# Performance work log

Hardware: AMD Instinct MI355X
Metric: run time of the kernel (lower is better)

The kernel has to match this reference:

```python
import jax, jax.numpy as jnp
import numpy as np

LAMBDA_SCR = 0.015
LAMBDA_IFD = 0.015


def setup_inputs() -> dict:
    key = jax.random.key(0)
    k = jax.random.split(key, 5)
    pred = jax.random.normal(k[0], (32, 1000), dtype=jnp.float32)
    feat0 = jax.random.normal(k[1], (32, 64, 128, 128), dtype=jnp.float32)
    feat1 = jax.random.normal(k[2], (32, 128, 64, 64), dtype=jnp.float32)
    feat2 = jax.random.normal(k[3], (32, 256, 32, 32), dtype=jnp.float32)  # teacher
    target = jax.random.randint(k[4], (32,), 0, 1000, dtype=jnp.int64)
    return {"pred": pred, "feat0": feat0, "feat1": feat1, "feat2": feat2, "target": target}


def _adaptive_avg_pool2d(x, out_hw):
    # Exact-multiple adaptive average pool (matches torch for integer ratios).
    B, C, H, W = x.shape
    Ho, Wo = out_hw
    if Ho >= H:
        x = jnp.repeat(x, Ho // H, axis=2)  # replication upsample
    else:
        x = x.reshape(B, C, Ho, H // Ho, W).mean(axis=3)
    if Wo >= W:
        x = jnp.repeat(x, Wo // W, axis=3)
    else:
        x = x.reshape(B, C, x.shape[2], Wo, W // Wo).mean(axis=4)
    return x


def _random_channel_selection(feat, target_channels, key):
    C = feat.shape[1]
    if C == target_channels:
        return feat
    idx = jax.random.permutation(key, C)[:target_channels]
    return feat[:, idx, :, :]


def _ifd_loss(feat):
    B, C, H, W = feat.shape
    if C < 2:
        return jnp.float32(0.0)
    # L2 norm per channel -> descending sort of channel indices
    norms = jnp.linalg.norm(feat.reshape(B, C, H * W), axis=-1)  # [B, C]
    idx = jnp.argsort(-norms, axis=1)                            # [B, C]
    half = C // 2
    strong = jnp.take_along_axis(feat, idx[:, :half, None, None], axis=1)
    weak = jnp.take_along_axis(feat, idx[:, half:2 * half, None, None], axis=1)
    A_strong = jax.nn.sigmoid(strong.mean(axis=1))  # [B, H, W]
    A_weak = jax.nn.sigmoid(weak.mean(axis=1))
    # sum_b mean_hw(diff^2) / B == mean over all elements
    return jnp.mean((A_weak - jax.lax.stop_gradient(A_strong)) ** 2)


def reference(pred, feat0, feat1, feat2, target):
    logp = jax.nn.log_softmax(pred, axis=-1)
    l_main = -jnp.mean(jnp.take_along_axis(logp, target[:, None], axis=1))

    features = [feat0, feat1, feat2]
    teacher = features[-1]
    students = features[:-1]

    sel_key = jax.random.key(42)  # fixed keys stand in for torch.randperm
    l_scr = jnp.float32(0.0)
    for i, student in enumerate(students):
        t_down = _adaptive_avg_pool2d(teacher, student.shape[2:])
        min_C = min(teacher.shape[1], student.shape[1])
        ks, kt = jax.random.split(jax.random.fold_in(sel_key, i))
        s_aligned = _random_channel_selection(student, min_C, ks)
        t_aligned = _random_channel_selection(t_down, min_C, kt)
        l_scr = l_scr + jnp.mean((s_aligned - jax.lax.stop_gradient(t_aligned)) ** 2)
    l_scr = l_scr / len(students)

    l_ifd = jnp.float32(0.0)
    for feat in features:
        l_ifd = l_ifd + _ifd_loss(feat)
    l_ifd = l_ifd / len(features)

    total = l_main + LAMBDA_SCR * l_scr + LAMBDA_IFD * l_ifd
    return (total, l_main, l_scr, l_ifd)
```

## Files before the change

### kernel.cpp

```cpp
#include <hip/hip_runtime.h>
#include <stdint.h>
#include <math.h>

#define NB 32

__device__ __forceinline__ void tf_block(uint32_t k0, uint32_t k1, uint32_t& x0, uint32_t& x1) {
  uint32_t k2 = 0x1BD11BDAu ^ k0 ^ k1;
  x0 += k0; x1 += k1;
#define TFR(r) { x0 += x1; x1 = (x1 << r) | (x1 >> (32 - r)); x1 ^= x0; }
  TFR(13) TFR(15) TFR(26) TFR(6)
  x0 += k1; x1 += k2 + 1u;
  TFR(17) TFR(29) TFR(16) TFR(24)
  x0 += k2; x1 += k0 + 2u;
  TFR(13) TFR(15) TFR(26) TFR(6)
  x0 += k0; x1 += k1 + 3u;
  TFR(17) TFR(29) TFR(16) TFR(24)
  x0 += k1; x1 += k2 + 4u;
  TFR(13) TFR(15) TFR(26) TFR(6)
  x0 += k2; x1 += k0 + 5u;
#undef TFR
}

__device__ __forceinline__ float sigmoidf(float x) { return 1.0f / (1.0f + expf(-x)); }

__device__ __forceinline__ float block_reduce(float v, float* red) {
  __syncthreads();
  int lane = threadIdx.x & 63, wv = threadIdx.x >> 6;
  for (int o = 32; o > 0; o >>= 1) v += __shfl_down(v, o, 64);
  if (lane == 0) red[wv] = v;
  __syncthreads();
  float r = 0.f;
  if (threadIdx.x == 0) r = red[0] + red[1] + red[2] + red[3];
  return r;
}

__global__ __launch_bounds__(256) void k0_perm(int* idx0, int* idx1, float* ws) {
  __shared__ uint32_t sub[2][2];
  __shared__ uint32_t bits[2][256];
  int t = threadIdx.x;
  for (int i = t; i < 384; i += 256) ws[i] = 0.0f;
  if (t == 0) {
    for (int i = 0; i < 2; ++i) {
      uint32_t f0 = 0u, f1 = (uint32_t)i;
      tf_block(0u, 42u, f0, f1);
      uint32_t a0 = 0u, a1 = 2u; tf_block(f0, f1, a0, a1);
      uint32_t b0 = 1u, b1 = 3u; tf_block(f0, f1, b0, b1);
      uint32_t kt0 = a1, kt1 = b1;
      uint32_t c0 = 0u, c1 = 2u; tf_block(kt0, kt1, c0, c1);
      uint32_t d0 = 1u, d1 = 3u; tf_block(kt0, kt1, d0, d1);
      sub[i][0] = c1; sub[i][1] = d1;
    }
  }
  __syncthreads();
  if (t < 128) {
    for (int i = 0; i < 2; ++i) {
      uint32_t x0 = (uint32_t)t, x1 = (uint32_t)(t + 128);
      tf_block(sub[i][0], sub[i][1], x0, x1);
      bits[i][t] = x0; bits[i][t + 128] = x1;
    }
  }
  __syncthreads();
  for (int i = 0; i < 2; ++i) {
    uint32_t mine = bits[i][t];
    int rank = 0;
    for (int k = 0; k < 256; ++k) {
      uint32_t v = bits[i][k];
      rank += (v < mine) || (v == mine && k < t);
    }
    int lim = (i == 0) ? 64 : 128;
    if (rank < lim) { (i == 0 ? idx0 : idx1)[rank] = t; }
  }
}

template<int C, int HW, int LOGW, int SHIFT, bool STUDENT>
__device__ __forceinline__ void pass1_work(const float* __restrict__ feat,
                                           const float* __restrict__ teacher,
                                           const int* __restrict__ tidx,
                                           float* __restrict__ normsq,
                                           float* __restrict__ scr_slots,
                                           int bc, float* tpl, float* red) {
  if constexpr (STUDENT) {
    int b = bc / C, c = bc % C;
    int tc = tidx[c];
    ((float4*)tpl)[threadIdx.x] =
        ((const float4*)(teacher + ((size_t)b * 256 + tc) * 1024))[threadIdx.x];
    __syncthreads();
  }
  const float4* plane = (const float4*)(feat + (size_t)bc * HW);
  float ssq = 0.f, scr = 0.f;
  for (int p = threadIdx.x; p < HW / 4; p += 256) {
    float4 v = plane[p];
    ssq += v.x * v.x + v.y * v.y + v.z * v.z + v.w * v.w;
    if constexpr (STUDENT) {
      int pix = p * 4;
      int h = pix >> LOGW;
      int w = pix & ((1 << LOGW) - 1);
      int th = h >> SHIFT;
      if constexpr (SHIFT == 2) {
        float tv = tpl[th * 32 + (w >> 2)];
        float dx = v.x - tv, dy = v.y - tv, dz = v.z - tv, dw = v.w - tv;
        scr += dx * dx + dy * dy + dz * dz + dw * dw;
      } else {
        int tw = w >> 1;
        float t0 = tpl[th * 32 + tw], t1 = tpl[th * 32 + tw + 1];
        float dx = v.x - t0, dy = v.y - t0, dz = v.z - t1, dw = v.w - t1;
        scr += dx * dx + dy * dy + dz * dz + dw * dw;
      }
    }
  }
  float r = block_reduce(ssq, red);
  if (threadIdx.x == 0) normsq[bc] = r;
  if constexpr (STUDENT) {
    float r2 = block_reduce(scr, red);
    if (threadIdx.x == 0) atomicAdd(&scr_slots[bc & 63], r2);
  }
}

__global__ __launch_bounds__(256) void k1_pass1(
    const float* __restrict__ f0, const float* __restrict__ f1, const float* __restrict__ f2,
    const int* __restrict__ idx0, const int* __restrict__ idx1,
    float* __restrict__ ns0, float* __restrict__ ns1, float* __restrict__ ns2,
    float* __restrict__ scr0_s, float* __restrict__ scr1_s) {
  __shared__ float tpl[1024];
  __shared__ float red[8];
  int bid = blockIdx.x;
  if (bid < 2048)       pass1_work<64, 16384, 7, 2, true >(f0, f2, idx0, ns0, scr0_s, bid,        tpl, red);
  else if (bid < 6144)  pass1_work<128, 4096, 6, 1, true >(f1, f2, idx1, ns1, scr1_s, bid - 2048, tpl, red);
  else                  pass1_work<256, 1024, 5, 0, false>(f2, nullptr, nullptr, ns2, nullptr, bid - 6144, tpl, red);
}

template<int C>
__device__ __forceinline__ void rank_work(const float* __restrict__ normsq,
                                          float* __restrict__ flags, int b, float* nm) {
  for (int c = threadIdx.x; c < C; c += 256) nm[c] = sqrtf(normsq[b * C + c]);
  __syncthreads();
  for (int c = threadIdx.x; c < C; c += 256) {
    float mine = nm[c];
    int rank = 0;
    for (int k = 0; k < C; ++k) {
      float v = nm[k];
      rank += (v > mine) || (v == mine && k < c);
    }
    flags[b * C + c] = (rank < C / 2) ? 1.0f : 0.0f;
  }
}

__device__ __forceinline__ void main_work(const float* __restrict__ pred,
                                          const int* __restrict__ target,
                                          float* acc, int b, float* sh) {
  int t = threadIdx.x;
  const float* row = pred + b * 1000;
  float m = -INFINITY;
  for (int j = t; j < 1000; j += 256) m = fmaxf(m, row[j]);
  sh[t] = m; __syncthreads();
  for (int s = 128; s > 0; s >>= 1) { if (t < s) sh[t] = fmaxf(sh[t], sh[t + s]); __syncthreads(); }
  m = sh[0]; __syncthreads();
  float e = 0.f;
  for (int j = t; j < 1000; j += 256) e += expf(row[j] - m);
  sh[t] = e; __syncthreads();
  for (int s = 128; s > 0; s >>= 1) { if (t < s) sh[t] += sh[t + s]; __syncthreads(); }
  if (t == 0) atomicAdd(acc, (logf(sh[0]) + m - row[target[b]]) * (1.0f / 32.0f));
}

__global__ __launch_bounds__(256) void k2_rank_main(
    const float* __restrict__ ns0, const float* __restrict__ ns1, const float* __restrict__ ns2,
    float* __restrict__ fl0, float* __restrict__ fl1, float* __restrict__ fl2,
    const float* __restrict__ pred, const int* __restrict__ target, float* main_acc) {
  __shared__ float sh[256];
  int bid = blockIdx.x;
  if (bid < 32)       rank_work<64 >(ns0, fl0, bid,      sh);
  else if (bid < 64)  rank_work<128>(ns1, fl1, bid - 32, sh);
  else if (bid < 96)  rank_work<256>(ns2, fl2, bid - 64, sh);
  else                main_work(pred, target, main_acc, bid - 96, sh);
}

template<int C, int HW>
__device__ __forceinline__ void pass2_vec4_work(const float* __restrict__ feat,
                                                const float* __restrict__ flags,
                                                float* __restrict__ slots, float inv_half,
                                                int bid, float* fl, float* red) {
  const int nchunk = HW / 1024;
  int b = bid / nchunk, chunk = bid % nchunk;
  for (int c = threadIdx.x; c < C; c += 256) fl[c] = flags[b * C + c];
  __syncthreads();
  const float* base = feat + (size_t)b * C * HW + (size_t)chunk * 1024;
  float4 tot = {0, 0, 0, 0}, str = {0, 0, 0, 0};
  for (int c = 0; c < C; ++c) {
    float4 v = ((const float4*)(base + (size_t)c * HW))[threadIdx.x];
    float f = fl[c];
    tot.x += v.x; tot.y += v.y; tot.z += v.z; tot.w += v.w;
    str.x = fmaf(v.x, f, str.x); str.y = fmaf(v.y, f, str.y);
    str.z = fmaf(v.z, f, str.z); str.w = fmaf(v.w, f, str.w);
  }
  float s = 0.f, d;
  d = sigmoidf((tot.x - str.x) * inv_half) - sigmoidf(str.x * inv_half); s += d * d;
  d = sigmoidf((tot.y - str.y) * inv_half) - sigmoidf(str.y * inv_half); s += d * d;
  d = sigmoidf((tot.z - str.z) * inv_half) - sigmoidf(str.z * inv_half); s += d * d;
  d = sigmoidf((tot.w - str.w) * inv_half) - sigmoidf(str.w * inv_half); s += d * d;
  float r = block_reduce(s, red);
  if (threadIdx.x == 0) atomicAdd(&slots[bid & 63], r);
}

__device__ __forceinline__ void pass2_feat2_work(const float* __restrict__ feat,
                                                 const float* __restrict__ flags,
                                                 float* __restrict__ slots, int bid,
                                                 float* fl, float* stot, float* sstr, float* red) {
  int b = bid >> 5, h = bid & 31;
  fl[threadIdx.x] = flags[b * 256 + threadIdx.x];
  __syncthreads();
  int w = threadIdx.x & 31;
  int cl = threadIdx.x >> 5;
  const float* base = feat + (size_t)b * 256 * 1024 + h * 32 + w;
  float tot = 0.f, str = 0.f;
  for (int cg = 0; cg < 32; ++cg) {
    int c = cg * 8 + cl;
    float v = base[(size_t)c * 1024];
    tot += v; str = fmaf(v, fl[c], str);
  }
  stot[threadIdx.x] = tot; sstr[threadIdx.x] = str;
  __syncthreads();
  float s = 0.f;
  if (threadIdx.x < 32) {
    float T = 0.f, S = 0.f;
    for (int k = 0; k < 8; ++k) { T += stot[k * 32 + threadIdx.x]; S += sstr[k * 32 + threadIdx.x]; }
    const float ih = 1.0f / 128.0f;
    float d = sigmoidf((T - S) * ih) - sigmoidf(S * ih);
    s = d * d;
  }
  float r = block_reduce(s, red);
  if (threadIdx.x == 0) atomicAdd(&slots[bid & 63], r);
}

__global__ __launch_bounds__(256) void k3_pass2(
    const float* __restrict__ f0, const float* __restrict__ f1, const float* __restrict__ f2,
    const float* __restrict__ fl0, const float* __restrict__ fl1, const float* __restrict__ fl2,
    float* __restrict__ ifd0_s, float* __restrict__ ifd1_s, float* __restrict__ ifd2_s) {
  __shared__ float fl[256];
  __shared__ float s1[256];
  __shared__ float s2[256];
  __shared__ float red[8];
  int bid = blockIdx.x;
  if (bid < 512)      pass2_vec4_work<64, 16384>(f0, fl0, ifd0_s, 1.0f / 32.0f, bid, fl, red);
  else if (bid < 640) pass2_vec4_work<128, 4096>(f1, fl1, ifd1_s, 1.0f / 64.0f, bid - 512, fl, red);
  else                pass2_feat2_work(f2, fl2, ifd2_s, bid - 640, fl, s1, s2, red);
}

__global__ void k4_finalize(const float* __restrict__ ws, float* __restrict__ out) {
  float scr0 = 0.f, scr1 = 0.f, ifd0 = 0.f, ifd1 = 0.f, ifd2 = 0.f;
  for (int i = 0; i < 64; ++i) {
    scr0 += ws[i];       scr1 += ws[64 + i];
    ifd0 += ws[128 + i]; ifd1 += ws[192 + i]; ifd2 += ws[256 + i];
  }
  float l_main = ws[320];
  scr0 *= (1.0f / (32.0f * 64.0f * 128.0f * 128.0f));
  scr1 *= (1.0f / (32.0f * 128.0f * 64.0f * 64.0f));
  float l_scr = 0.5f * (scr0 + scr1);
  ifd0 *= (1.0f / (32.0f * 128.0f * 128.0f));
  ifd1 *= (1.0f / (32.0f * 64.0f * 64.0f));
  ifd2 *= (1.0f / (32.0f * 32.0f * 32.0f));
  float l_ifd = (ifd0 + ifd1 + ifd2) * (1.0f / 3.0f);
  float total = l_main + 0.015f * l_scr + 0.015f * l_ifd;
  out[0] = total; out[1] = l_main; out[2] = l_scr; out[3] = l_ifd;
}

extern "C" void kernel_launch(void* const* d_in, const int* in_sizes, int n_in,
                              void* d_out, int out_size, void* d_ws, size_t ws_size,
                              hipStream_t stream) {
  (void)in_sizes; (void)n_in; (void)out_size; (void)ws_size;
  const float* pred   = (const float*)d_in[0];
  const float* feat0  = (const float*)d_in[1];
  const float* feat1  = (const float*)d_in[2];
  const float* feat2  = (const float*)d_in[3];
  const int*   target = (const int*)d_in[4];
  float* out = (float*)d_out;

  float* ws = (float*)d_ws;
  float* scr0_s = ws;
  float* scr1_s = ws + 64;
  float* ifd0_s = ws + 128;
  float* ifd1_s = ws + 192;
  float* ifd2_s = ws + 256;
  float* main_a = ws + 320;
  int*   idx0 = (int*)(ws + 384);
  int*   idx1 = idx0 + 64;
  float* ns0  = (float*)(idx1 + 128);
  float* ns1  = ns0 + 2048;
  float* ns2  = ns1 + 4096;
  float* fl0  = ns2 + 8192;
  float* fl1  = fl0 + 2048;
  float* fl2  = fl1 + 4096;

  k0_perm<<<1, 256, 0, stream>>>(idx0, idx1, ws);
  k1_pass1<<<14336, 256, 0, stream>>>(feat0, feat1, feat2, idx0, idx1, ns0, ns1, ns2, scr0_s, scr1_s);
  k2_rank_main<<<128, 256, 0, stream>>>(ns0, ns1, ns2, fl0, fl1, fl2, pred, target, main_a);
  k3_pass2<<<1664, 256, 0, stream>>>(feat0, feat1, feat2, fl0, fl1, fl2, ifd0_s, ifd1_s, ifd2_s);
  k4_finalize<<<1, 1, 0, stream>>>(ws, out);
}
```

Baseline: 334.9 us.

## Restructure passes: spatial-chunk blocks, store channel totals, gather only weak channels

Pass 1 is reorganised so each block covers a spatial chunk across all channels. It writes per-chunk partial channel norms via wave shuffles and stores the per-pixel channel sum to workspace. The rank kernel now emits the list of weak-channel indices instead of a 0/1 flag array. Pass 2 then gathers only the weak half of the channels and reuses the stored totals, so it reads roughly half the feature data. The cost is extra workspace writes for the totals, far fewer blocks (704 instead of 14336), and a fallback path that keeps the full-channel loop when the workspace is too small.

```diff
diff --git a/kernel.cpp b/kernel.cpp
--- a/kernel.cpp
+++ b/kernel.cpp
@@ -72,76 +72,136 @@
   }
 }
 
-template<int C, int HW, int LOGW, int SHIFT, bool STUDENT>
-__device__ __forceinline__ void pass1_work(const float* __restrict__ feat,
-                                           const float* __restrict__ teacher,
-                                           const int* __restrict__ tidx,
-                                           float* __restrict__ normsq,
-                                           float* __restrict__ scr_slots,
-                                           int bc, float* tpl, float* red) {
-  if constexpr (STUDENT) {
-    int b = bc / C, c = bc % C;
-    int tc = tidx[c];
-    ((float4*)tpl)[threadIdx.x] =
-        ((const float4*)(teacher + ((size_t)b * 256 + tc) * 1024))[threadIdx.x];
-    __syncthreads();
-  }
-  const float4* plane = (const float4*)(feat + (size_t)bc * HW);
-  float ssq = 0.f, scr = 0.f;
-  for (int p = threadIdx.x; p < HW / 4; p += 256) {
-    float4 v = plane[p];
-    ssq += v.x * v.x + v.y * v.y + v.z * v.z + v.w * v.w;
-    if constexpr (STUDENT) {
-      int pix = p * 4;
-      int h = pix >> LOGW;
-      int w = pix & ((1 << LOGW) - 1);
-      int th = h >> SHIFT;
-      if constexpr (SHIFT == 2) {
-        float tv = tpl[th * 32 + (w >> 2)];
-        float dx = v.x - tv, dy = v.y - tv, dz = v.z - tv, dw = v.w - tv;
-        scr += dx * dx + dy * dy + dz * dz + dw * dw;
-      } else {
-        int tw = w >> 1;
-        float t0 = tpl[th * 32 + tw], t1 = tpl[th * 32 + tw + 1];
-        float dx = v.x - t0, dy = v.y - t0, dz = v.z - t1, dw = v.w - t1;
-        scr += dx * dx + dy * dy + dz * dz + dw * dw;
-      }
-    }
-  }
-  float r = block_reduce(ssq, red);
-  if (threadIdx.x == 0) normsq[bc] = r;
-  if constexpr (STUDENT) {
-    float r2 = block_reduce(scr, red);
-    if (threadIdx.x == 0) atomicAdd(&scr_slots[bc & 63], r2);
-  }
-}
-
+
+template<bool WT>
+__device__ __forceinline__ void p1_feat2(const float* __restrict__ f2,
+                                         float* __restrict__ ns2p, float* __restrict__ tot2,
+                                         int q, float* nsp, int lane, int wv) {
+  int b = q >> 1, hf = q & 1;
+  int t = threadIdx.x;
+  const float2* base = (const float2*)(f2 + (size_t)b * 262144 + hf * 512);
+  float2 tot = {0.f, 0.f};
+  #pragma unroll 4
+  for (int c = 0; c < 256; ++c) {
+    float2 v = base[c * 512 + t];
+    tot.x += v.x; tot.y += v.y;
+    float s = v.x * v.x + v.y * v.y;
+    #pragma unroll
+    for (int o = 32; o > 0; o >>= 1) s += __shfl_down(s, o, 64);
+    if (lane == 0) nsp[c * 4 + wv] = s;
+  }
+  __syncthreads();
+  ns2p[(b * 2 + hf) * 256 + t] = nsp[4 * t] + nsp[4 * t + 1] + nsp[4 * t + 2] + nsp[4 * t + 3];
+  if (WT) ((float2*)(tot2 + b * 1024 + hf * 512))[t] = tot;
+}
+
+template<bool WT>
+__device__ __forceinline__ void p1_feat1(const float* __restrict__ f1, const float* __restrict__ f2,
+                                         const int* __restrict__ idx1,
+                                         float* __restrict__ ns1p, float* __restrict__ scr1_s,
+                                         float* __restrict__ tot1,
+                                         int q, float* nsp, int* sidx, float* red, int lane, int wv) {
+  int b = q >> 2, chunk = q & 3;
+  int t = threadIdx.x;
+  if (t < 128) sidx[t] = idx1[t];
+  __syncthreads();
+  const float4* base = (const float4*)(f1 + (size_t)b * 524288 + chunk * 1024);
+  int th = chunk * 8 + (t >> 5);
+  const float* tbase = f2 + (size_t)b * 262144 + th * 32 + (t & 15) * 2;
+  float4 tot = {0.f, 0.f, 0.f, 0.f};
+  float scr = 0.f;
+  #pragma unroll 4
+  for (int c = 0; c < 128; ++c) {
+    float4 v = base[c * 1024 + t];
+    float2 tv = *(const float2*)(tbase + (size_t)sidx[c] * 1024);
+    tot.x += v.x; tot.y += v.y; tot.z += v.z; tot.w += v.w;
+    float s = v.x * v.x + v.y * v.y + v.z * v.z + v.w * v.w;
+    float dx = v.x - tv.x, dy = v.y - tv.x, dz = v.z - tv.y, dw = v.w - tv.y;
+    scr += dx * dx + dy * dy + dz * dz + dw * dw;
+    #pragma unroll
+    for (int o = 32; o > 0; o >>= 1) s += __shfl_down(s, o, 64);
+    if (lane == 0) nsp[c * 4 + wv] = s;
+  }
+  __syncthreads();
+  if (t < 128) ns1p[(b * 4 + chunk) * 128 + t] =
+      nsp[4 * t] + nsp[4 * t + 1] + nsp[4 * t + 2] + nsp[4 * t + 3];
+  if (WT) ((float4*)(tot1 + (size_t)b * 4096 + chunk * 1024))[t] = tot;
+  float r = block_reduce(scr, red);
+  if (t == 0) atomicAdd(&scr1_s[q & 63], r);
+}
+
+template<bool WT>
+__device__ __forceinline__ void p1_feat0(const float* __restrict__ f0, const float* __restrict__ f2,
+                                         const int* __restrict__ idx0,
+                                         float* __restrict__ ns0p, float* __restrict__ scr0_s,
+                                         float* __restrict__ tot0,
+                                         int q, float* nsp, int* sidx, float* red, int lane, int wv) {
+  int b = q >> 4, chunk = q & 15;
+  int t = threadIdx.x;
+  if (t < 64) sidx[t] = idx0[t];
+  __syncthreads();
+  const float4* base = (const float4*)(f0 + (size_t)b * 1048576 + chunk * 1024);
+  int th = chunk * 2 + (t >> 7);
+  const float* tbase = f2 + (size_t)b * 262144 + th * 32 + (t & 31);
+  float4 tot = {0.f, 0.f, 0.f, 0.f};
+  float scr = 0.f;
+  #pragma unroll 4
+  for (int c = 0; c < 64; ++c) {
+    float4 v = base[c * 4096 + t];
+    float tv = tbase[(size_t)sidx[c] * 1024];
+    tot.x += v.x; tot.y += v.y; tot.z += v.z; tot.w += v.w;
+    float s = v.x * v.x + v.y * v.y + v.z * v.z + v.w * v.w;
+    float dx = v.x - tv, dy = v.y - tv, dz = v.z - tv, dw = v.w - tv;
+    scr += dx * dx + dy * dy + dz * dz + dw * dw;
+    #pragma unroll
+    for (int o = 32; o > 0; o >>= 1) s += __shfl_down(s, o, 64);
+    if (lane == 0) nsp[c * 4 + wv] = s;
+  }
+  __syncthreads();
+  if (t < 64) ns0p[(b * 16 + chunk) * 64 + t] =
+      nsp[4 * t] + nsp[4 * t + 1] + nsp[4 * t + 2] + nsp[4 * t + 3];
+  if (WT) ((float4*)(tot0 + (size_t)b * 16384 + chunk * 1024))[t] = tot;
+  float r = block_reduce(scr, red);
+  if (t == 0) atomicAdd(&scr0_s[q & 63], r);
+}
+
+template<bool WT>
 __global__ __launch_bounds__(256) void k1_pass1(
     const float* __restrict__ f0, const float* __restrict__ f1, const float* __restrict__ f2,
     const int* __restrict__ idx0, const int* __restrict__ idx1,
-    float* __restrict__ ns0, float* __restrict__ ns1, float* __restrict__ ns2,
-    float* __restrict__ scr0_s, float* __restrict__ scr1_s) {
-  __shared__ float tpl[1024];
+    float* __restrict__ ns0p, float* __restrict__ ns1p, float* __restrict__ ns2p,
+    float* __restrict__ scr0_s, float* __restrict__ scr1_s,
+    float* __restrict__ tot0, float* __restrict__ tot1, float* __restrict__ tot2) {
+  __shared__ float nsp[1024];
+  __shared__ int sidx[128];
   __shared__ float red[8];
   int bid = blockIdx.x;
-  if (bid < 2048)       pass1_work<64, 16384, 7, 2, true >(f0, f2, idx0, ns0, scr0_s, bid,        tpl, red);
-  else if (bid < 6144)  pass1_work<128, 4096, 6, 1, true >(f1, f2, idx1, ns1, scr1_s, bid - 2048, tpl, red);
-  else                  pass1_work<256, 1024, 5, 0, false>(f2, nullptr, nullptr, ns2, nullptr, bid - 6144, tpl, red);
-}
-
-template<int C>
-__device__ __forceinline__ void rank_work(const float* __restrict__ normsq,
-                                          float* __restrict__ flags, int b, float* nm) {
-  for (int c = threadIdx.x; c < C; c += 256) nm[c] = sqrtf(normsq[b * C + c]);
-  __syncthreads();
-  for (int c = threadIdx.x; c < C; c += 256) {
-    float mine = nm[c];
+  int lane = threadIdx.x & 63, wv = threadIdx.x >> 6;
+  if (bid < 64)       p1_feat2<WT>(f2, ns2p, tot2, bid, nsp, lane, wv);
+  else if (bid < 192) p1_feat1<WT>(f1, f2, idx1, ns1p, scr1_s, tot1, bid - 64, nsp, sidx, red, lane, wv);
+  else                p1_feat0<WT>(f0, f2, idx0, ns0p, scr0_s, tot0, bid - 192, nsp, sidx, red, lane, wv);
+}
+
+template<int C, int NP>
+__device__ __forceinline__ void rank_work(const float* __restrict__ nspg,
+                                          int* __restrict__ widx, int b, float* nm) {
+  int t = threadIdx.x;
+  if (t < C) {
+    float s = 0.f;
+    #pragma unroll
+    for (int p = 0; p < NP; ++p) s += nspg[(b * NP + p) * C + t];
+    nm[t] = sqrtf(s);
+  }
+  __syncthreads();
+  if (t < C) {
+    float mine = nm[t];
     int rank = 0;
     for (int k = 0; k < C; ++k) {
       float v = nm[k];
-      rank += (v > mine) || (v == mine && k < c);
-    }
-    flags[b * C + c] = (rank < C / 2) ? 1.0f : 0.0f;
+      rank += (v > mine) || (v == mine && k < t);
+    }
+    constexpr int HALF = C / 2;
+    if (rank >= HALF) widx[b * HALF + rank - HALF] = t;
   }
 }
 
@@ -163,86 +223,116 @@
 }
 
 __global__ __launch_bounds__(256) void k2_rank_main(
-    const float* __restrict__ ns0, const float* __restrict__ ns1, const float* __restrict__ ns2,
-    float* __restrict__ fl0, float* __restrict__ fl1, float* __restrict__ fl2,
-    const float* __restrict__ pred, const int* __restrict__ target, float* main_acc) {
+    const float* __restrict__ ns0p, const float* __restrict__ ns1p, const float* __restrict__ ns2p,
+    int* __restrict__ widx0, int* __restrict__ widx1, int* __restrict__ widx2,
+    const float* __restrict__ pred, const int* __restrict__ target, float* __restrict__ main_acc) {
   __shared__ float sh[256];
   int bid = blockIdx.x;
-  if (bid < 32)       rank_work<64 >(ns0, fl0, bid,      sh);
-  else if (bid < 64)  rank_work<128>(ns1, fl1, bid - 32, sh);
-  else if (bid < 96)  rank_work<256>(ns2, fl2, bid - 64, sh);
+  if (bid < 32)       rank_work<64, 16>(ns0p, widx0, bid, sh);
+  else if (bid < 64)  rank_work<128, 4>(ns1p, widx1, bid - 32, sh);
+  else if (bid < 96)  rank_work<256, 2>(ns2p, widx2, bid - 64, sh);
   else                main_work(pred, target, main_acc, bid - 96, sh);
 }
 
-template<int C, int HW>
-__device__ __forceinline__ void pass2_vec4_work(const float* __restrict__ feat,
-                                                const float* __restrict__ flags,
-                                                float* __restrict__ slots, float inv_half,
-                                                int bid, float* fl, float* red) {
-  const int nchunk = HW / 1024;
-  int b = bid / nchunk, chunk = bid % nchunk;
-  for (int c = threadIdx.x; c < C; c += 256) fl[c] = flags[b * C + c];
-  __syncthreads();
-  const float* base = feat + (size_t)b * C * HW + (size_t)chunk * 1024;
-  float4 tot = {0, 0, 0, 0}, str = {0, 0, 0, 0};
-  for (int c = 0; c < C; ++c) {
-    float4 v = ((const float4*)(base + (size_t)c * HW))[threadIdx.x];
-    float f = fl[c];
-    tot.x += v.x; tot.y += v.y; tot.z += v.z; tot.w += v.w;
-    str.x = fmaf(v.x, f, str.x); str.y = fmaf(v.y, f, str.y);
-    str.z = fmaf(v.z, f, str.z); str.w = fmaf(v.w, f, str.w);
+template<int C, int NCHUNK, bool WT>
+__device__ __forceinline__ void ifd_vec4(const float* __restrict__ feat,
+                                         const int* __restrict__ widx,
+                                         const float* __restrict__ tot,
+                                         float* __restrict__ slots,
+                                         int q, int* swx, float* wf, float* red) {
+  constexpr int HALF = C / 2;
+  constexpr int HW = NCHUNK * 1024;
+  const float ih = 1.0f / (float)HALF;
+  int b = q / NCHUNK, chunk = q % NCHUNK;
+  int t = threadIdx.x;
+  const float4* base = (const float4*)(feat + (size_t)b * C * HW + chunk * 1024);
+  float4 wk = {0.f, 0.f, 0.f, 0.f};
+  float4 tt = {0.f, 0.f, 0.f, 0.f};
+  if (WT) {
+    if (t < HALF) swx[t] = widx[b * HALF + t];
+    __syncthreads();
+    #pragma unroll 4
+    for (int i = 0; i < HALF; ++i) {
+      float4 v = base[swx[i] * (HW / 4) + t];
+      wk.x += v.x; wk.y += v.y; wk.z += v.z; wk.w += v.w;
+    }
+    tt = ((const float4*)(tot + (size_t)b * HW + chunk * 1024))[t];
+  } else {
+    for (int c = t; c < C; c += 256) wf[c] = 0.f;
+    __syncthreads();
+    if (t < HALF) wf[widx[b * HALF + t]] = 1.f;
+    __syncthreads();
+    #pragma unroll 2
+    for (int c = 0; c < C; ++c) {
+      float4 v = base[c * (HW / 4) + t];
+      float f = wf[c];
+      tt.x += v.x; tt.y += v.y; tt.z += v.z; tt.w += v.w;
+      wk.x = fmaf(v.x, f, wk.x); wk.y = fmaf(v.y, f, wk.y);
+      wk.z = fmaf(v.z, f, wk.z); wk.w = fmaf(v.w, f, wk.w);
+    }
   }
   float s = 0.f, d;
-  d = sigmoidf((tot.x - str.x) * inv_half) - sigmoidf(str.x * inv_half); s += d * d;
-  d = sigmoidf((tot.y - str.y) * inv_half) - sigmoidf(str.y * inv_half); s += d * d;
-  d = sigmoidf((tot.z - str.z) * inv_half) - sigmoidf(str.z * inv_half); s += d * d;
-  d = sigmoidf((tot.w - str.w) * inv_half) - sigmoidf(str.w * inv_half); s += d * d;
+  d = sigmoidf(wk.x * ih) - sigmoidf((tt.x - wk.x) * ih); s += d * d;
+  d = sigmoidf(wk.y * ih) - sigmoidf((tt.y - wk.y) * ih); s += d * d;
+  d = sigmoidf(wk.z * ih) - sigmoidf((tt.z - wk.z) * ih); s += d * d;
+  d = sigmoidf(wk.w * ih) - sigmoidf((tt.w - wk.w) * ih); s += d * d;
   float r = block_reduce(s, red);
-  if (threadIdx.x == 0) atomicAdd(&slots[bid & 63], r);
-}
-
-__device__ __forceinline__ void pass2_feat2_work(const float* __restrict__ feat,
-                                                 const float* __restrict__ flags,
-                                                 float* __restrict__ slots, int bid,
-                                                 float* fl, float* stot, float* sstr, float* red) {
-  int b = bid >> 5, h = bid & 31;
-  fl[threadIdx.x] = flags[b * 256 + threadIdx.x];
-  __syncthreads();
-  int w = threadIdx.x & 31;
-  int cl = threadIdx.x >> 5;
-  const float* base = feat + (size_t)b * 256 * 1024 + h * 32 + w;
-  float tot = 0.f, str = 0.f;
-  for (int cg = 0; cg < 32; ++cg) {
-    int c = cg * 8 + cl;
-    float v = base[(size_t)c * 1024];
-    tot += v; str = fmaf(v, fl[c], str);
-  }
-  stot[threadIdx.x] = tot; sstr[threadIdx.x] = str;
-  __syncthreads();
-  float s = 0.f;
-  if (threadIdx.x < 32) {
-    float T = 0.f, S = 0.f;
-    for (int k = 0; k < 8; ++k) { T += stot[k * 32 + threadIdx.x]; S += sstr[k * 32 + threadIdx.x]; }
-    const float ih = 1.0f / 128.0f;
-    float d = sigmoidf((T - S) * ih) - sigmoidf(S * ih);
-    s = d * d;
-  }
+  if (t == 0) atomicAdd(&slots[q & 63], r);
+}
+
+template<bool WT>
+__device__ __forceinline__ void ifd_feat2(const float* __restrict__ f2,
+                                          const int* __restrict__ widx2,
+                                          const float* __restrict__ tot2,
+                                          float* __restrict__ slots,
+                                          int q, int* swx, float* wf, float* red) {
+  int b = q >> 1, hf = q & 1;
+  int t = threadIdx.x;
+  const float ih = 1.0f / 128.0f;
+  const float2* base = (const float2*)(f2 + (size_t)b * 262144 + hf * 512);
+  float2 wk = {0.f, 0.f}, tt = {0.f, 0.f};
+  if (WT) {
+    if (t < 128) swx[t] = widx2[b * 128 + t];
+    __syncthreads();
+    #pragma unroll 4
+    for (int i = 0; i < 128; ++i) {
+      float2 v = base[swx[i] * 512 + t];
+      wk.x += v.x; wk.y += v.y;
+    }
+    tt = ((const float2*)(tot2 + b * 1024 + hf * 512))[t];
+  } else {
+    wf[t] = 0.f;
+    __syncthreads();
+    if (t < 128) wf[widx2[b * 128 + t]] = 1.f;
+    __syncthreads();
+    #pragma unroll 2
+    for (int c = 0; c < 256; ++c) {
+      float2 v = base[c * 512 + t];
+      float f = wf[c];
+      tt.x += v.x; tt.y += v.y;
+      wk.x = fmaf(v.x, f, wk.x); wk.y = fmaf(v.y, f, wk.y);
+    }
+  }
+  float s = 0.f, d;
+  d = sigmoidf(wk.x * ih) - sigmoidf((tt.x - wk.x) * ih); s += d * d;
+  d = sigmoidf(wk.y * ih) - sigmoidf((tt.y - wk.y) * ih); s += d * d;
   float r = block_reduce(s, red);
-  if (threadIdx.x == 0) atomicAdd(&slots[bid & 63], r);
-}
-
+  if (t == 0) atomicAdd(&slots[q & 63], r);
+}
+
+template<bool WT>
 __global__ __launch_bounds__(256) void k3_pass2(
     const float* __restrict__ f0, const float* __restrict__ f1, const float* __restrict__ f2,
-    const float* __restrict__ fl0, const float* __restrict__ fl1, const float* __restrict__ fl2,
+    const int* __restrict__ widx0, const int* __restrict__ widx1, const int* __restrict__ widx2,
+    const float* __restrict__ tot0, const float* __restrict__ tot1, const float* __restrict__ tot2,
     float* __restrict__ ifd0_s, float* __restrict__ ifd1_s, float* __restrict__ ifd2_s) {
-  __shared__ float fl[256];
-  __shared__ float s1[256];
-  __shared__ float s2[256];
+  __shared__ int swx[128];
+  __shared__ float wf[256];
   __shared__ float red[8];
   int bid = blockIdx.x;
-  if (bid < 512)      pass2_vec4_work<64, 16384>(f0, fl0, ifd0_s, 1.0f / 32.0f, bid, fl, red);
-  else if (bid < 640) pass2_vec4_work<128, 4096>(f1, fl1, ifd1_s, 1.0f / 64.0f, bid - 512, fl, red);
-  else                pass2_feat2_work(f2, fl2, ifd2_s, bid - 640, fl, s1, s2, red);
+  if (bid < 64)       ifd_feat2<WT>(f2, widx2, tot2, ifd2_s, bid, swx, wf, red);
+  else if (bid < 192) ifd_vec4<128, 4, WT>(f1, widx1, tot1, ifd1_s, bid - 64, swx, wf, red);
+  else                ifd_vec4<64, 16, WT>(f0, widx0, tot0, ifd0_s, bid - 192, swx, wf, red);
 }
 
 __global__ void k4_finalize(const float* __restrict__ ws, float* __restrict__ out) {
@@ -266,7 +356,7 @@
 extern "C" void kernel_launch(void* const* d_in, const int* in_sizes, int n_in,
                               void* d_out, int out_size, void* d_ws, size_t ws_size,
                               hipStream_t stream) {
-  (void)in_sizes; (void)n_in; (void)out_size; (void)ws_size;
+  (void)in_sizes; (void)n_in; (void)out_size;
   const float* pred   = (const float*)d_in[0];
   const float* feat0  = (const float*)d_in[1];
   const float* feat1  = (const float*)d_in[2];
@@ -274,25 +364,41 @@
   const int*   target = (const int*)d_in[4];
   float* out = (float*)d_out;
 
-  float* ws = (float*)d_ws;
+  float* ws     = (float*)d_ws;
   float* scr0_s = ws;
   float* scr1_s = ws + 64;
   float* ifd0_s = ws + 128;
   float* ifd1_s = ws + 192;
   float* ifd2_s = ws + 256;
-  float* main_a = ws + 320;
-  int*   idx0 = (int*)(ws + 384);
-  int*   idx1 = idx0 + 64;
-  float* ns0  = (float*)(idx1 + 128);
-  float* ns1  = ns0 + 2048;
-  float* ns2  = ns1 + 4096;
-  float* fl0  = ns2 + 8192;
-  float* fl1  = fl0 + 2048;
-  float* fl2  = fl1 + 4096;
+  int*   idx0   = (int*)(ws + 384);
+  int*   idx1   = idx0 + 64;
+  int*   widx0  = idx1 + 128;
+  int*   widx1  = widx0 + 1024;
+  int*   widx2  = widx1 + 2048;
+  float* ns0p   = (float*)(widx2 + 4096);
+  float* ns1p   = ns0p + 32768;
+  float* ns2p   = ns1p + 16384;
+  float* tot0   = ns2p + 16384;
+  float* tot1   = tot0 + 524288;
+  float* tot2   = tot1 + 131072;
+  const size_t need_full = (size_t)761408 * 4;
+  bool wt = (ws_size == 0) || (ws_size >= need_full);
 
   k0_perm<<<1, 256, 0, stream>>>(idx0, idx1, ws);
-  k1_pass1<<<14336, 256, 0, stream>>>(feat0, feat1, feat2, idx0, idx1, ns0, ns1, ns2, scr0_s, scr1_s);
-  k2_rank_main<<<128, 256, 0, stream>>>(ns0, ns1, ns2, fl0, fl1, fl2, pred, target, main_a);
-  k3_pass2<<<1664, 256, 0, stream>>>(feat0, feat1, feat2, fl0, fl1, fl2, ifd0_s, ifd1_s, ifd2_s);
+  if (wt) {
+    k1_pass1<true><<<704, 256, 0, stream>>>(feat0, feat1, feat2, idx0, idx1,
+                                            ns0p, ns1p, ns2p, scr0_s, scr1_s, tot0, tot1, tot2);
+    k2_rank_main<<<128, 256, 0, stream>>>(ns0p, ns1p, ns2p, widx0, widx1, widx2,
+                                          pred, target, ws + 320);
+    k3_pass2<true><<<704, 256, 0, stream>>>(feat0, feat1, feat2, widx0, widx1, widx2,
+                                            tot0, tot1, tot2, ifd0_s, ifd1_s, ifd2_s);
+  } else {
+    k1_pass1<false><<<704, 256, 0, stream>>>(feat0, feat1, feat2, idx0, idx1,
+                                             ns0p, ns1p, ns2p, scr0_s, scr1_s, tot0, tot1, tot2);
+    k2_rank_main<<<128, 256, 0, stream>>>(ns0p, ns1p, ns2p, widx0, widx1, widx2,
+                                          pred, target, ws + 320);
+    k3_pass2<false><<<704, 256, 0, stream>>>(feat0, feat1, feat2, widx0, widx1, widx2,
+                                             tot0, tot1, tot2, ifd0_s, ifd1_s, ifd2_s);
+  }
   k4_finalize<<<1, 1, 0, stream>>>(ws, out);
 }
```

New measurement: 410.7 us. +22.6%, slower.
